# Optimization experiments

Hardware: AMD Instinct MI355X
Metric: run time of the kernel (lower is better)

Reference implementation:

```python
import jax, jax.numpy as jnp
import numpy as np

NR, NQ, NH, NV = 256, 64, 64, 4
B = 8192
NDRAW = 12
# zoneout probabilities from __init__ (applied deterministically, eval-mode expectation)
ZO_IJ, ZO_ID, ZO_GJ, ZO_GD = 0.3, 0.2, 0.3, 0.2


def _lin_init(key, fan_in, fan_out):
    kw, kb = jax.random.split(key)
    s = 1.0 / np.sqrt(fan_in)
    W = jax.random.uniform(kw, (fan_in, fan_out), jnp.float32, -s, s)
    b = jax.random.uniform(kb, (fan_out,), jnp.float32, -s, s)
    return W, b


def setup_inputs() -> dict:
    key = jax.random.key(0)
    ks = jax.random.split(key, 16)
    inp = {"ndraw": NDRAW}
    inp["cnd_repr"] = jax.random.normal(ks[0], (B, NR), jnp.float32)
    inp["qry_jrep"] = jax.random.normal(ks[1], (B, NQ), jnp.float32)
    inp["qry_drep"] = jax.random.normal(ks[2], (B, NQ), jnp.float32)
    inp["qry_v"] = jax.random.normal(ks[3], (B, NV), jnp.float32)
    for n in ["hi_j", "ci_j", "oi_j", "hi_d", "ci_d", "oi_d",
              "hg_j", "cg_j", "og_j", "hg_d", "cg_d", "og_d", "ug_j", "ug_d"]:
        inp[n] = jnp.zeros((B, NH), jnp.float32)
    # LSTM cells: W [in+nh, 4*nh]
    inp["W_ij"], inp["b_ij"] = _lin_init(ks[4], NR + NQ + NH + NH, 4 * NH)
    inp["W_id"], inp["b_id"] = _lin_init(ks[5], NR + NQ + NH + NH, 4 * NH)
    inp["W_gj"], inp["b_gj"] = _lin_init(ks[6], NR + NH + NH, 4 * NH)
    inp["W_gd"], inp["b_gd"] = _lin_init(ks[7], NR + NH + NV + NH, 4 * NH)
    # GaussianFactor heads: nh -> (mean, logv)
    inp["W_poj"], inp["b_poj"] = _lin_init(ks[8], NH, 2 * NH)
    inp["W_pod"], inp["b_pod"] = _lin_init(ks[9], NH, 2 * NH)
    inp["W_prj"], inp["b_prj"] = _lin_init(ks[10], NH, 2 * NH)
    inp["W_prd"], inp["b_prd"] = _lin_init(ks[11], NH, 2 * NH)
    # GeneratorDelta: cat(u, h) -> delta
    inp["W_dj"], inp["b_dj"] = _lin_init(ks[12], 2 * NH, NH)
    inp["W_dd"], inp["b_dd"] = _lin_init(ks[13], 2 * NH, NH)
    return inp


def _lstm(x, h, c, W, b, zo):
    g = jnp.concatenate([x, h], axis=1) @ W + b  # [B, 4*NH]
    i, f, gg, o = jnp.split(g, 4, axis=1)
    i, f, o = jax.nn.sigmoid(i), jax.nn.sigmoid(f), jax.nn.sigmoid(o)
    c_new = f * c + i * jnp.tanh(gg)
    h_new = o * jnp.tanh(c_new)
    # deterministic zoneout (expectation form)
    return zo * h + (1.0 - zo) * h_new, zo * c + (1.0 - zo) * c_new, o


def _gauss_stats(h, W, b):
    s = h @ W + b
    mean, logv = jnp.split(s, 2, axis=1)
    return mean, logv


def _delta(u, h, W, b):
    return jax.nn.leaky_relu(jnp.concatenate([u, h], axis=1) @ W + b)


def _forward(ndraw, cnd_repr, qry_jrep, qry_drep, qry_v,
             hi_j, ci_j, oi_j, hi_d, ci_d, oi_d,
             hg_j, cg_j, og_j, hg_d, cg_d, og_d, ug_j, ug_d,
             W_ij, b_ij, W_id, b_id, W_gj, b_gj, W_gd, b_gd,
             W_poj, b_poj, W_pod, b_pod, W_prj, b_prj, W_prd, b_prd,
             W_dj, b_dj, W_dd, b_dd):
    Bn = cnd_repr.shape[0]
    eps_j = jax.random.normal(jax.random.key(1), (ndraw, Bn, NH), jnp.float32)
    eps_d = jax.random.normal(jax.random.key(2), (ndraw, Bn, NH), jnp.float32)

    def step(carry, eps):
        (hi_j, ci_j, oi_j, hi_d, ci_d, oi_d,
         hg_j, cg_j, og_j, hg_d, cg_d, og_d, ug_j, ug_d) = carry
        ej, ed = eps
        # priors from current generator states (sampled z unused in loop)
        pr_m_j, pr_v_j = _gauss_stats(hg_j, W_prj, b_prj)
        pr_m_d, pr_v_d = _gauss_stats(hg_d, W_prd, b_prd)
        # inference states
        inp_ij = jnp.concatenate([cnd_repr, qry_jrep, hg_j], axis=1)
        inp_id = jnp.concatenate([cnd_repr, qry_drep, hg_d], axis=1)
        hi_j, ci_j, oi_j = _lstm(inp_ij, hi_j, ci_j, W_ij, b_ij, ZO_IJ)
        hi_d, ci_d, oi_d = _lstm(inp_id, hi_d, ci_d, W_id, b_id, ZO_ID)
        # posteriors + reparameterized samples
        po_m_j, po_v_j = _gauss_stats(hi_j, W_poj, b_poj)
        po_m_d, po_v_d = _gauss_stats(hi_d, W_pod, b_pod)
        z_j = po_m_j + jnp.exp(0.5 * po_v_j) * ej
        z_d = po_m_d + jnp.exp(0.5 * po_v_d) * ed
        # generator states
        inp_gj = jnp.concatenate([cnd_repr, z_j], axis=1)
        inp_gd = jnp.concatenate([cnd_repr, z_d, qry_v], axis=1)
        hg_j, cg_j, og_j = _lstm(inp_gj, hg_j, cg_j, W_gj, b_gj, ZO_GJ)
        hg_d, cg_d, og_d = _lstm(inp_gd, hg_d, cg_d, W_gd, b_gd, ZO_GD)
        # additive canvas updates
        ug_j = ug_j + _delta(ug_j, hg_j, W_dj, b_dj)
        ug_d = ug_d + _delta(ug_d, hg_d, W_dd, b_dd)
        carry = (hi_j, ci_j, oi_j, hi_d, ci_d, oi_d,
                 hg_j, cg_j, og_j, hg_d, cg_d, og_d, ug_j, ug_d)
        ys = (pr_m_j, pr_v_j, pr_m_d, pr_v_d, po_m_j, po_v_j, po_m_d, po_v_d)
        return carry, ys

    carry0 = (hi_j, ci_j, oi_j, hi_d, ci_d, oi_d,
              hg_j, cg_j, og_j, hg_d, cg_d, og_d, ug_j, ug_d)
    carry, ys = jax.lax.scan(step, carry0, (eps_j, eps_d))
    ug_j_out, ug_d_out = carry[-2], carry[-1]
    # pack: [2 + 8*ndraw, B, NH] (canvases then per-draw prior/posterior stats)
    out = jnp.concatenate([ug_j_out[None], ug_d_out[None]] + list(ys), axis=0)
    return out


def reference(ndraw, cnd_repr, qry_jrep, qry_drep, qry_v,
              hi_j, ci_j, oi_j, hi_d, ci_d, oi_d,
              hg_j, cg_j, og_j, hg_d, cg_d, og_d, ug_j, ug_d,
              W_ij, b_ij, W_id, b_id, W_gj, b_gj, W_gd, b_gd,
              W_poj, b_poj, W_pod, b_pod, W_prj, b_prj, W_prd, b_prd,
              W_dj, b_dj, W_dd, b_dd):
    return _forward(ndraw, cnd_repr, qry_jrep, qry_drep, qry_v,
                    hi_j, ci_j, oi_j, hi_d, ci_d, oi_d,
                    hg_j, cg_j, og_j, hg_d, cg_d, og_d, ug_j, ug_d,
                    W_ij, b_ij, W_id, b_id, W_gj, b_gj, W_gd, b_gd,
                    W_poj, b_poj, W_pod, b_pod, W_prj, b_prj, W_prd, b_prd,
                    W_dj, b_dj, W_dd, b_dd)
```

## Files before the change

kernel.cpp:

```cpp
#include <hip/hip_runtime.h>
#include <hip/hip_bf16.h>


typedef __attribute__((ext_vector_type(8))) short bf16x8;
typedef __attribute__((ext_vector_type(4))) float f32x4;

#define MFMA(A, Bv, C) __builtin_amdgcn_mfma_f32_16x16x32_bf16(A, Bv, C, 0, 0, 0)

#define FR_WI   0
#define FR_WG   32768
#define FR_WPR  65536
#define FR_WPO  73728
#define FR_WD   81920
#define FR_SIDE 90112

__device__ __forceinline__ unsigned short f2bf(float f) {
  unsigned u = __float_as_uint(f);
  return (unsigned short)((u + 0x7FFFu + ((u >> 16) & 1u)) >> 16);
}
__device__ __forceinline__ unsigned pk2(float a, float b) {
  return (unsigned)f2bf(a) | ((unsigned)f2bf(b) << 16);
}
__device__ __forceinline__ float sigf(float x) {
  return 1.0f / (1.0f + __expf(-x));
}
__device__ __forceinline__ float tanh_f(float x) {
  return 1.0f - 2.0f / (__expf(2.0f * x) + 1.0f);
}

__device__ __forceinline__ float eps_threefry(unsigned seed, unsigned idx) {
  unsigned x0 = 0u, x1 = idx;
  const unsigned ks0 = 0u, ks1 = seed, ks2 = seed ^ 0x1BD11BDAu;
  x0 += ks0; x1 += ks1;
#define TF_R(r) { x0 += x1; x1 = (x1 << (r)) | (x1 >> (32 - (r))); x1 ^= x0; }
  TF_R(13) TF_R(15) TF_R(26) TF_R(6)  x0 += ks1; x1 += ks2 + 1u;
  TF_R(17) TF_R(29) TF_R(16) TF_R(24) x0 += ks2; x1 += ks0 + 2u;
  TF_R(13) TF_R(15) TF_R(26) TF_R(6)  x0 += ks0; x1 += ks1 + 3u;
  TF_R(17) TF_R(29) TF_R(16) TF_R(24) x0 += ks1; x1 += ks2 + 4u;
  TF_R(13) TF_R(15) TF_R(26) TF_R(6)  x0 += ks2; x1 += ks0 + 5u;
#undef TF_R
  unsigned bits = x0 ^ x1;
  unsigned fb = (bits >> 9) | 0x3F800000u;
  const float lo = -0.99999994f;
  float f = __uint_as_float(fb) - 1.0f;
  float u = fmaxf(lo, f * 2.0f + lo);
  float w = -log1pf(-u * u);
  float p;
  if (w < 5.0f) {
    w -= 2.5f;
    p = 2.81022636e-08f;
    p = fmaf(p, w, 3.43273939e-07f);
    p = fmaf(p, w, -3.5233877e-06f);
    p = fmaf(p, w, -4.39150654e-06f);
    p = fmaf(p, w, 0.00021858087f);
    p = fmaf(p, w, -0.00125372503f);
    p = fmaf(p, w, -0.00417768164f);
    p = fmaf(p, w, 0.246640727f);
    p = fmaf(p, w, 1.50140941f);
  } else {
    w = sqrtf(w) - 3.0f;
    p = -0.000200214257f;
    p = fmaf(p, w, 0.000100950558f);
    p = fmaf(p, w, 0.00134934322f);
    p = fmaf(p, w, -0.00367342844f);
    p = fmaf(p, w, 0.00573950773f);
    p = fmaf(p, w, -0.0076224613f);
    p = fmaf(p, w, 0.00943887047f);
    p = fmaf(p, w, 1.00167406f);
    p = fmaf(p, w, 2.83297682f);
  }
  return 1.41421356f * (p * u);
}

__global__ __launch_bounds__(256) void GeRN_prepEps(
    const float* __restrict__ Wij, const float* __restrict__ Wid,
    const float* __restrict__ Wgj, const float* __restrict__ Wgd,
    const float* __restrict__ Wprj, const float* __restrict__ Wprd,
    const float* __restrict__ Wpoj, const float* __restrict__ Wpod,
    const float* __restrict__ Wdj, const float* __restrict__ Wdd,
    unsigned short* __restrict__ frB, unsigned short* __restrict__ sBs,
    float* __restrict__ ebuf, unsigned ndBN)
{
  if (blockIdx.x < 236) {
    const int vb = blockIdx.x * 4 + (threadIdx.x >> 6);
    const int l = threadIdx.x & 63;
    if (vb < 352) {
      const int s = vb / 176;
      int tt = vb % 176;
      const float* W; int ldw, rb, NT, kt, nt; size_t doff;
      if (tt < 64)       { W = s ? Wid : Wij; ldw = 256; NT = 16; kt = tt >> 4; nt = tt & 15;
                           rb = 320 + kt * 32; doff = FR_WI; }
      else if (tt < 128) { tt -= 64; W = s ? Wgd : Wgj; ldw = 256; NT = 16; kt = tt >> 4; nt = tt & 15;
                           rb = (kt < 2) ? 256 + kt * 32 : (s ? 324 : 320) + (kt - 2) * 32; doff = FR_WG; }
      else if (tt < 144) { tt -= 128; W = s ? Wprd : Wprj; ldw = 128; NT = 8; kt = tt >> 3; nt = tt & 7;
                           rb = kt * 32; doff = FR_WPR; }
      else if (tt < 160) { tt -= 144; W = s ? Wpod : Wpoj; ldw = 128; NT = 8; kt = tt >> 3; nt = tt & 7;
                           rb = kt * 32; doff = FR_WPO; }
      else               { tt -= 160; W = s ? Wdd : Wdj; ldw = 64; NT = 4; kt = tt >> 2; nt = tt & 3;
                           rb = (kt < 2) ? kt * 32 : 64 + (kt - 2) * 32; doff = FR_WD; }
      unsigned short* dst = frB + (size_t)s * FR_SIDE + doff
                          + ((size_t)(kt * NT + nt) * 64 + l) * 8;
      const int kk = (l >> 4) * 8;
      const int c = nt * 16 + (l & 15);
      #pragma unroll
      for (int j = 0; j < 8; ++j)
        dst[j] = f2bf(W[(size_t)(rb + kk + j) * ldw + c]);
    } else {
      int bb = vb - 352;
      int mat, base;
      if (bb < 160)      { mat = 0; base = 0; }
      else if (bb < 320) { mat = 1; base = 160; }
      else if (bb < 448) { mat = 2; base = 320; }
      else               { mat = 3; base = 448; }
      int tt = bb - base;
      int kk = tt >> 4, nt = tt & 15;
      const float* W = mat == 0 ? Wij : mat == 1 ? Wid : mat == 2 ? Wgj : Wgd;
      const int c = nt * 16 + (l & 15);
      const int kl0 = (l >> 4) * 8;
      unsigned short* dst = sBs + ((size_t)bb * 64 + l) * 8;
      if (mat == 3 && kk == 8) {
        #pragma unroll
        for (int j = 0; j < 8; ++j) {
          int klo = kl0 + j;
          dst[j] = (klo < 4) ? f2bf(W[(size_t)(320 + klo) * 256 + c]) : (unsigned short)0;
        }
      } else {
        int rb = (kk < 8) ? kk * 32 : 256 + (kk - 8) * 32;
        #pragma unroll
        for (int j = 0; j < 8; ++j)
          dst[j] = f2bf(W[(size_t)(rb + kl0 + j) * 256 + c]);
      }
    }
  } else {
    unsigned j0 = ((blockIdx.x - 236) * 256u + threadIdx.x) * 8u;
    const unsigned total = 2u * ndBN;
    if (j0 >= total) return;
    const unsigned s = (j0 >= ndBN) ? 1u : 0u;
    const unsigned i0 = j0 - s * ndBN;
    const unsigned seed = 1u + s;
    float v[8];
    #pragma unroll
    for (int k = 0; k < 8; ++k) v[k] = eps_threefry(seed, i0 + (unsigned)k);
    float4 a = {v[0], v[1], v[2], v[3]};
    float4 b = {v[4], v[5], v[6], v[7]};
    *(float4*)(ebuf + j0) = a;
    *(float4*)(ebuf + j0 + 4) = b;
  }
}

#define WR_FR(buf, row, c, v) \
  fr[rh][buf][(c) >> 5][((row) & 15) + (((c) >> 3) & 3) * 16][(c) & 7] = f2bf(v)
#define LD_FR(buf, kt) (*(const bf16x8*)&fr[rh][buf][kt][l][0])
#define LD_B(off, kt, nt, NT) \
  (*(const bf16x8*)(FB + (off) + (((kt) * (NT) + (nt)) * 64 + l) * 8))
#define LD_S(idx) (*(const bf16x8*)&sBs[((size_t)(idx) * 64 + l) * 8])
#define LD_WI(kt, nt) (*(const bf16x8*)&wiL[(((kt) * 16 + (nt)) * 64 + l) * 8])
#define LD_WG(kt, nt) (*(const bf16x8*)&wgL[(((kt) * 16 + (nt)) * 64 + l) * 8])
#define LD_A(kt) (*(const bf16x8*)&AsBuf[(((size_t)rh * 11 + (kt)) * 64 + l) * 8])

template<int USE_EPS>
__global__ __launch_bounds__(512, 2) void GeRN_recur(
    const unsigned short* __restrict__ frB,
    const unsigned short* __restrict__ sBs,
    const float* __restrict__ cnd, const float* __restrict__ qjg,
    const float* __restrict__ qdg, const float* __restrict__ qvg,
    const float* __restrict__ bij, const float* __restrict__ bid,
    const float* __restrict__ bgj, const float* __restrict__ bgd,
    const float* __restrict__ bprj, const float* __restrict__ bprd,
    const float* __restrict__ bpoj, const float* __restrict__ bpod,
    const float* __restrict__ bdj,  const float* __restrict__ bdd,
    const float* __restrict__ hi_j0, const float* __restrict__ ci_j0,
    const float* __restrict__ hi_d0, const float* __restrict__ ci_d0,
    const float* __restrict__ hg_j0, const float* __restrict__ cg_j0,
    const float* __restrict__ hg_d0, const float* __restrict__ cg_d0,
    const float* __restrict__ ug_j0, const float* __restrict__ ug_d0,
    const float* __restrict__ eps_buf, unsigned ndBN,
    float* __restrict__ out, int B, int nd)
{
  alignas(16) __shared__ unsigned short fr[2][6][2][64][8];
  alignas(16) __shared__ unsigned short wiL[32768];
  alignas(16) __shared__ unsigned short wgL[32768];
  unsigned short* AsBuf = wgL;

  const int tid = threadIdx.x;
  const int l   = tid & 63;
  const int w   = tid >> 6;
  const int rh  = w >> 2;
  const int ws  = w & 3;
  const int s   = blockIdx.x & 1;
  const int rbk = blockIdx.x >> 1;
  const int r0  = (l >> 4) * 4;
  const int col = ws * 16 + (l & 15);
  const int bbase = rbk * 32 + rh * 16;
  const int bblk  = rbk * 32;
  const size_t BN = (size_t)B * 64;

  const float* hi0 = s ? hi_d0 : hi_j0;  const float* ci0 = s ? ci_d0 : ci_j0;
  const float* hg0 = s ? hg_d0 : hg_j0;  const float* cg0 = s ? cg_d0 : cg_j0;
  const float* ug0 = s ? ug_d0 : ug_j0;
  const float* BPR = s ? bprd : bprj;
  const float* BPO = s ? bpod : bpoj;
  const float* BD  = s ? bdd  : bdj;
  const float* BI  = s ? bid  : bij;
  const float* BG  = s ? bgd  : bgj;
  const float* qq  = s ? qdg  : qjg;
  const unsigned short* FB = frB + (size_t)s * FR_SIDE;

  for (int i = tid; i < 32 * 44; i += 512) {
    int r = i / 44, kc = i % 44;
    int rhh = r >> 4, rr = r & 15;
    float v[8];
    if (kc < 32) {
      const float4* p = (const float4*)&cnd[(size_t)(bblk + r) * 256 + kc * 8];
      float4 x0 = p[0], x1 = p[1];
      v[0] = x0.x; v[1] = x0.y; v[2] = x0.z; v[3] = x0.w;
      v[4] = x1.x; v[5] = x1.y; v[6] = x1.z; v[7] = x1.w;
    } else if (kc < 40) {
      const float4* p = (const float4*)&qq[(size_t)(bblk + r) * 64 + (kc - 32) * 8];
      float4 x0 = p[0], x1 = p[1];
      v[0] = x0.x; v[1] = x0.y; v[2] = x0.z; v[3] = x0.w;
      v[4] = x1.x; v[5] = x1.y; v[6] = x1.z; v[7] = x1.w;
    } else if (kc == 40 && s) {
      #pragma unroll
      for (int j = 0; j < 8; ++j) v[j] = (j < 4) ? qvg[(size_t)(bblk + r) * 4 + j] : 0.0f;
    } else {
      #pragma unroll
      for (int j = 0; j < 8; ++j) v[j] = 0.0f;
    }
    int kt = kc >> 2;
    int lane = rr + (kc & 3) * 16;
    uint4 wq;
    wq.x = pk2(v[0], v[1]); wq.y = pk2(v[2], v[3]);
    wq.z = pk2(v[4], v[5]); wq.w = pk2(v[6], v[7]);
    *(uint4*)&AsBuf[(((size_t)rhh * 11 + kt) * 64 + lane) * 8] = wq;
  }
  __syncthreads();

  f32x4 preI[4], preG[4];
  {
    const int ktB_I = s ? 160 : 0;
    const int ktB_G = s ? 448 : 320;
    const int ktN_G = s ? 9 : 8;
    #pragma unroll
    for (int g = 0; g < 4; ++g) {
      float bi = BI[g * 64 + col];
      float bg = BG[g * 64 + col];
      f32x4 vi = {bi, bi, bi, bi};
      f32x4 vg = {bg, bg, bg, bg};
      preI[g] = vi; preG[g] = vg;
    }
    #pragma unroll
    for (int kk = 0; kk < 10; ++kk) {
      bf16x8 a = LD_A(kk);
      #pragma unroll
      for (int g = 0; g < 4; ++g)
        preI[g] = MFMA(a, LD_S(ktB_I + kk * 16 + g * 4 + ws), preI[g]);
    }
    for (int kk = 0; kk < ktN_G; ++kk) {
      int ktA = (kk < 8) ? kk : 10;
      bf16x8 a = LD_A(ktA);
      #pragma unroll
      for (int g = 0; g < 4; ++g)
        preG[g] = MFMA(a, LD_S(ktB_G + kk * 16 + g * 4 + ws), preG[g]);
    }
  }

  float hi_[4], ci_[4], hg_[4], cg_[4], u_[4];
  #pragma unroll
  for (int r = 0; r < 4; ++r) {
    size_t gi = (size_t)(bbase + r0 + r) * 64 + col;
    hi_[r] = hi0[gi]; ci_[r] = ci0[gi];
    hg_[r] = hg0[gi]; cg_[r] = cg0[gi];
    u_[r]  = ug0[gi];
  }
  const float bprm = BPR[col], bprv = BPR[64 + col];
  const float bpom = BPO[col], bpov = BPO[64 + col];
  const float bd   = BD[col];

  #pragma unroll
  for (int r = 0; r < 4; ++r) {
    WR_FR(0, r0 + r, col, hi_[r]);
    WR_FR(2, r0 + r, col, hg_[r]);
    WR_FR(4, r0 + r, col, u_[r]);
  }
  __syncthreads();

  {
    const uint4* srcI = (const uint4*)(FB + FR_WI);
    uint4* dI = (uint4*)wiL;
    for (int i = tid; i < 4096; i += 512) dI[i] = srcI[i];
    const uint4* srcG = (const uint4*)(FB + FR_WG);
    uint4* dG = (uint4*)wgL;
    for (int i = tid; i < 4096; i += 512) dG[i] = srcG[i];
  }
  __syncthreads();

  const float zo = s ? 0.2f : 0.3f, zo1 = 1.0f - zo;

  const unsigned gi0 = (unsigned)((bbase + r0) * 64 + col);
  float* o_prm = out + (size_t)(2 + (2 * s) * nd) * BN + gi0;
  float* o_prv = out + (size_t)(2 + (2 * s + 1) * nd) * BN + gi0;
  float* o_pom = out + (size_t)(2 + (4 + 2 * s) * nd) * BN + gi0;
  float* o_pov = out + (size_t)(2 + (5 + 2 * s) * nd) * BN + gi0;
  unsigned e0 = gi0;
  const unsigned BNu = (unsigned)BN;
  const unsigned eseed = 1u + (unsigned)s;
  const float* ep = USE_EPS ? (eps_buf + (size_t)s * ndBN + gi0) : (const float*)0;

  for (int t = 0; t < nd; ++t) {
    const int cb = t & 1;
    float epre[4];
    if (USE_EPS) {
      #pragma unroll
      for (int r = 0; r < 4; ++r) epre[r] = ep[r * 64];
    }
    bf16x8 a_hg0 = LD_FR(2, 0), a_hg1 = LD_FR(2, 1);
    bf16x8 a_hi0 = LD_FR(cb, 0), a_hi1 = LD_FR(cb, 1);

    {
      f32x4 am = {bprm, bprm, bprm, bprm};
      f32x4 av = {bprv, bprv, bprv, bprv};
      am = MFMA(a_hg0, LD_B(FR_WPR, 0, ws, 8), am);
      am = MFMA(a_hg1, LD_B(FR_WPR, 1, ws, 8), am);
      av = MFMA(a_hg0, LD_B(FR_WPR, 0, ws + 4, 8), av);
      av = MFMA(a_hg1, LD_B(FR_WPR, 1, ws + 4, 8), av);
      #pragma unroll
      for (int r = 0; r < 4; ++r) {
        o_prm[r * 64] = am[r];
        o_prv[r * 64] = av[r];
      }
    }
    {
      f32x4 acc[4];
      #pragma unroll
      for (int g = 0; g < 4; ++g) acc[g] = preI[g];
      #pragma unroll
      for (int g = 0; g < 4; ++g) {
        acc[g] = MFMA(a_hg0, LD_WI(0, g * 4 + ws), acc[g]);
        acc[g] = MFMA(a_hg1, LD_WI(1, g * 4 + ws), acc[g]);
        acc[g] = MFMA(a_hi0, LD_WI(2, g * 4 + ws), acc[g]);
        acc[g] = MFMA(a_hi1, LD_WI(3, g * 4 + ws), acc[g]);
      }
      #pragma unroll
      for (int r = 0; r < 4; ++r) {
        float ig = sigf(acc[0][r]), fg = sigf(acc[1][r]);
        float gg = tanh_f(acc[2][r]), og = sigf(acc[3][r]);
        float cn = fmaf(fg, ci_[r], ig * gg);
        float hn = og * tanh_f(cn);
        hi_[r] = fmaf(zo, hi_[r], zo1 * hn);
        ci_[r] = fmaf(zo, ci_[r], zo1 * cn);
        WR_FR(cb ^ 1, r0 + r, col, hi_[r]);
      }
    }
    __syncthreads();

    {
      bf16x8 a0 = LD_FR(cb ^ 1, 0), a1 = LD_FR(cb ^ 1, 1);
      f32x4 am = {bpom, bpom, bpom, bpom};
      f32x4 av = {bpov, bpov, bpov, bpov};
      am = MFMA(a0, LD_B(FR_WPO, 0, ws, 8), am);
      am = MFMA(a1, LD_B(FR_WPO, 1, ws, 8), am);
      av = MFMA(a0, LD_B(FR_WPO, 0, ws + 4, 8), av);
      av = MFMA(a1, LD_B(FR_WPO, 1, ws + 4, 8), av);
      #pragma unroll
      for (int r = 0; r < 4; ++r) {
        o_pom[r * 64] = am[r];
        o_pov[r * 64] = av[r];
        float e = USE_EPS ? epre[r] : eps_threefry(eseed, e0 + r * 64);
        float z = fmaf(__expf(0.5f * av[r]), e, am[r]);
        WR_FR(3, r0 + r, col, z);
      }
    }
    __syncthreads();

    {
      bf16x8 az0 = LD_FR(3, 0), az1 = LD_FR(3, 1);
      f32x4 acc[4];
      #pragma unroll
      for (int g = 0; g < 4; ++g) acc[g] = preG[g];
      #pragma unroll
      for (int g = 0; g < 4; ++g) {
        acc[g] = MFMA(az0,   LD_WG(0, g * 4 + ws), acc[g]);
        acc[g] = MFMA(az1,   LD_WG(1, g * 4 + ws), acc[g]);
        acc[g] = MFMA(a_hg0, LD_WG(2, g * 4 + ws), acc[g]);
        acc[g] = MFMA(a_hg1, LD_WG(3, g * 4 + ws), acc[g]);
      }
      #pragma unroll
      for (int r = 0; r < 4; ++r) {
        float ig = sigf(acc[0][r]), fg = sigf(acc[1][r]);
        float gg = tanh_f(acc[2][r]), og = sigf(acc[3][r]);
        float cn = fmaf(fg, cg_[r], ig * gg);
        float hn = og * tanh_f(cn);
        hg_[r] = fmaf(zo, hg_[r], zo1 * hn);
        cg_[r] = fmaf(zo, cg_[r], zo1 * cn);
        WR_FR(2, r0 + r, col, hg_[r]);
      }
    }
    __syncthreads();

    {
      bf16x8 au0 = LD_FR(4 + cb, 0), au1 = LD_FR(4 + cb, 1);
      bf16x8 ah0 = LD_FR(2, 0), ah1 = LD_FR(2, 1);
      f32x4 acc = {bd, bd, bd, bd};
      acc = MFMA(au0, LD_B(FR_WD, 0, ws, 4), acc);
      acc = MFMA(au1, LD_B(FR_WD, 1, ws, 4), acc);
      acc = MFMA(ah0, LD_B(FR_WD, 2, ws, 4), acc);
      acc = MFMA(ah1, LD_B(FR_WD, 3, ws, 4), acc);
      #pragma unroll
      for (int r = 0; r < 4; ++r) {
        float a = acc[r];
        float d = a > 0.0f ? a : 0.01f * a;
        u_[r] += d;
        WR_FR(4 + (cb ^ 1), r0 + r, col, u_[r]);
      }
    }
    __syncthreads();

    o_prm += BN; o_prv += BN; o_pom += BN; o_pov += BN;
    e0 += BNu;
    if (USE_EPS) ep += BN;
  }

  #pragma unroll
  for (int r = 0; r < 4; ++r) {
    size_t gi = (size_t)(bbase + r0 + r) * 64 + col;
    out[(size_t)s * BN + gi] = u_[r];
  }
}

extern "C" void kernel_launch(void* const* d_in, const int* in_sizes, int n_in,
                              void* d_out, int out_size, void* d_ws, size_t ws_size,
                              hipStream_t stream)
{
  const float* cnd = (const float*)d_in[1];
  const float* qj  = (const float*)d_in[2];
  const float* qd  = (const float*)d_in[3];
  const float* qv  = (const float*)d_in[4];
  const float* hi_j0 = (const float*)d_in[5];
  const float* ci_j0 = (const float*)d_in[6];
  const float* hi_d0 = (const float*)d_in[8];
  const float* ci_d0 = (const float*)d_in[9];
  const float* hg_j0 = (const float*)d_in[11];
  const float* cg_j0 = (const float*)d_in[12];
  const float* hg_d0 = (const float*)d_in[14];
  const float* cg_d0 = (const float*)d_in[15];
  const float* ug_j0 = (const float*)d_in[17];
  const float* ug_d0 = (const float*)d_in[18];
  const float* Wij = (const float*)d_in[19]; const float* bij = (const float*)d_in[20];
  const float* Wid = (const float*)d_in[21]; const float* bid = (const float*)d_in[22];
  const float* Wgj = (const float*)d_in[23]; const float* bgj = (const float*)d_in[24];
  const float* Wgd = (const float*)d_in[25]; const float* bgd = (const float*)d_in[26];
  const float* Wpoj = (const float*)d_in[27]; const float* bpoj = (const float*)d_in[28];
  const float* Wpod = (const float*)d_in[29]; const float* bpod = (const float*)d_in[30];
  const float* Wprj = (const float*)d_in[31]; const float* bprj = (const float*)d_in[32];
  const float* Wprd = (const float*)d_in[33]; const float* bprd = (const float*)d_in[34];
  const float* Wdj = (const float*)d_in[35]; const float* bdj = (const float*)d_in[36];
  const float* Wdd = (const float*)d_in[37]; const float* bdd = (const float*)d_in[38];

  const int B = in_sizes[1] / 256;
  const int slots = out_size / (B * 64);
  const int nd = (slots - 2) / 8;

  unsigned short* frB = (unsigned short*)d_ws;
  unsigned short* sBs = frB + 2 * FR_SIDE;
  size_t epsOff = (size_t)2 * FR_SIDE * 2 + (size_t)592 * 512 * 2;
  epsOff = (epsOff + 255) & ~(size_t)255;
  const unsigned ndBN = (unsigned)((size_t)nd * B * 64);
  float* epsBuf = (float*)((char*)d_ws + epsOff);
  const bool useEps = ws_size >= epsOff + (size_t)2 * ndBN * 4;
  float* out = (float*)d_out;

  const int epsBlocks = useEps ? (int)((2u * ndBN + 2047u) / 2048u) : 0;
  GeRN_prepEps<<<236 + epsBlocks, 256, 0, stream>>>(
      Wij, Wid, Wgj, Wgd, Wprj, Wprd, Wpoj, Wpod, Wdj, Wdd, frB, sBs,
      epsBuf, ndBN);
  if (useEps) {
    GeRN_recur<1><<<2 * (B / 32), 512, 0, stream>>>(
        frB, sBs, cnd, qj, qd, qv, bij, bid, bgj, bgd,
        bprj, bprd, bpoj, bpod, bdj, bdd,
        hi_j0, ci_j0, hi_d0, ci_d0, hg_j0, cg_j0, hg_d0, cg_d0, ug_j0, ug_d0,
        epsBuf, ndBN, out, B, nd);
  } else {
    GeRN_recur<0><<<2 * (B / 32), 512, 0, stream>>>(
        frB, sBs, cnd, qj, qd, qv, bij, bid, bgj, bgd,
        bprj, bprd, bpoj, bpod, bdj, bdd,
        hi_j0, ci_j0, hi_d0, ci_d0, hg_j0, cg_j0, hg_d0, cg_d0, ug_j0, ug_d0,
        (const float*)0, ndBN, out, B, nd);
  }
}
```

Measured before the change: 191.2 us.

## Process 64 batch rows per block with two column tiles per wave

```diff
diff --git a/kernel.cpp b/kernel.cpp
--- a/kernel.cpp
+++ b/kernel.cpp
@@ -149,14 +149,14 @@
 }
 
 #define WR_FR(buf, row, c, v) \
-  fr[rh][buf][(c) >> 5][((row) & 15) + (((c) >> 3) & 3) * 16][(c) & 7] = f2bf(v)
-#define LD_FR(buf, kt) (*(const bf16x8*)&fr[rh][buf][kt][l][0])
+  fr[rq][buf][(c) >> 5][((row) & 15) + (((c) >> 3) & 3) * 16][(c) & 7] = f2bf(v)
+#define LD_FR(buf, kt) (*(const bf16x8*)&fr[rq][buf][kt][l][0])
 #define LD_B(off, kt, nt, NT) \
   (*(const bf16x8*)(FB + (off) + (((kt) * (NT) + (nt)) * 64 + l) * 8))
 #define LD_S(idx) (*(const bf16x8*)&sBs[((size_t)(idx) * 64 + l) * 8])
 #define LD_WI(kt, nt) (*(const bf16x8*)&wiL[(((kt) * 16 + (nt)) * 64 + l) * 8])
 #define LD_WG(kt, nt) (*(const bf16x8*)&wgL[(((kt) * 16 + (nt)) * 64 + l) * 8])
-#define LD_A(kt) (*(const bf16x8*)&AsBuf[(((size_t)rh * 11 + (kt)) * 64 + l) * 8])
+#define LD_A(kt) (*(const bf16x8*)&AsBuf[(((size_t)rq * 11 + (kt)) * 64 + l) * 8])
 
 template<int USE_EPS>
 __global__ __launch_bounds__(512, 2) void GeRN_recur(
@@ -177,7 +177,7 @@
     const float* __restrict__ eps_buf, unsigned ndBN,
     float* __restrict__ out, int B, int nd)
 {
-  alignas(16) __shared__ unsigned short fr[2][6][2][64][8];
+  alignas(16) __shared__ unsigned short fr[4][4][2][64][8];
   alignas(16) __shared__ unsigned short wiL[32768];
   alignas(16) __shared__ unsigned short wgL[32768];
   unsigned short* AsBuf = wgL;
@@ -185,14 +185,14 @@
   const int tid = threadIdx.x;
   const int l   = tid & 63;
   const int w   = tid >> 6;
-  const int rh  = w >> 2;
-  const int ws  = w & 3;
+  const int rq  = w >> 1;
+  const int ws  = w & 1;
   const int s   = blockIdx.x & 1;
   const int rbk = blockIdx.x >> 1;
   const int r0  = (l >> 4) * 4;
-  const int col = ws * 16 + (l & 15);
-  const int bbase = rbk * 32 + rh * 16;
-  const int bblk  = rbk * 32;
+  const int col0 = ws * 32 + (l & 15);
+  const int bbase = rbk * 64 + rq * 16;
+  const int bblk  = rbk * 64;
   const size_t BN = (size_t)B * 64;
 
   const float* hi0 = s ? hi_d0 : hi_j0;  const float* ci0 = s ? ci_d0 : ci_j0;
@@ -206,9 +206,9 @@
   const float* qq  = s ? qdg  : qjg;
   const unsigned short* FB = frB + (size_t)s * FR_SIDE;
 
-  for (int i = tid; i < 32 * 44; i += 512) {
+  for (int i = tid; i < 64 * 44; i += 512) {
     int r = i / 44, kc = i % 44;
-    int rhh = r >> 4, rr = r & 15;
+    int rqq = r >> 4, rr = r & 15;
     float v[8];
     if (kc < 32) {
       const float4* p = (const float4*)&cnd[(size_t)(bblk + r) * 256 + kc * 8];
@@ -232,57 +232,71 @@
     uint4 wq;
     wq.x = pk2(v[0], v[1]); wq.y = pk2(v[2], v[3]);
     wq.z = pk2(v[4], v[5]); wq.w = pk2(v[6], v[7]);
-    *(uint4*)&AsBuf[(((size_t)rhh * 11 + kt) * 64 + lane) * 8] = wq;
+    *(uint4*)&AsBuf[(((size_t)rqq * 11 + kt) * 64 + lane) * 8] = wq;
   }
   __syncthreads();
 
-  f32x4 preI[4], preG[4];
+  f32x4 preI[4][2], preG[4][2];
   {
     const int ktB_I = s ? 160 : 0;
     const int ktB_G = s ? 448 : 320;
     const int ktN_G = s ? 9 : 8;
     #pragma unroll
-    for (int g = 0; g < 4; ++g) {
-      float bi = BI[g * 64 + col];
-      float bg = BG[g * 64 + col];
-      f32x4 vi = {bi, bi, bi, bi};
-      f32x4 vg = {bg, bg, bg, bg};
-      preI[g] = vi; preG[g] = vg;
-    }
+    for (int g = 0; g < 4; ++g)
+      #pragma unroll
+      for (int c = 0; c < 2; ++c) {
+        float bi = BI[g * 64 + col0 + c * 16];
+        float bg = BG[g * 64 + col0 + c * 16];
+        f32x4 vi = {bi, bi, bi, bi};
+        f32x4 vg = {bg, bg, bg, bg};
+        preI[g][c] = vi; preG[g][c] = vg;
+      }
     #pragma unroll
     for (int kk = 0; kk < 10; ++kk) {
       bf16x8 a = LD_A(kk);
       #pragma unroll
       for (int g = 0; g < 4; ++g)
-        preI[g] = MFMA(a, LD_S(ktB_I + kk * 16 + g * 4 + ws), preI[g]);
+        #pragma unroll
+        for (int c = 0; c < 2; ++c)
+          preI[g][c] = MFMA(a, LD_S(ktB_I + kk * 16 + g * 4 + ws * 2 + c), preI[g][c]);
     }
     for (int kk = 0; kk < ktN_G; ++kk) {
       int ktA = (kk < 8) ? kk : 10;
       bf16x8 a = LD_A(ktA);
       #pragma unroll
       for (int g = 0; g < 4; ++g)
-        preG[g] = MFMA(a, LD_S(ktB_G + kk * 16 + g * 4 + ws), preG[g]);
-    }
-  }
-
-  float hi_[4], ci_[4], hg_[4], cg_[4], u_[4];
+        #pragma unroll
+        for (int c = 0; c < 2; ++c)
+          preG[g][c] = MFMA(a, LD_S(ktB_G + kk * 16 + g * 4 + ws * 2 + c), preG[g][c]);
+    }
+  }
+
+  float hi_[2][4], ci_[2][4], hg_[2][4], cg_[2][4], u_[2][4];
   #pragma unroll
-  for (int r = 0; r < 4; ++r) {
-    size_t gi = (size_t)(bbase + r0 + r) * 64 + col;
-    hi_[r] = hi0[gi]; ci_[r] = ci0[gi];
-    hg_[r] = hg0[gi]; cg_[r] = cg0[gi];
-    u_[r]  = ug0[gi];
-  }
-  const float bprm = BPR[col], bprv = BPR[64 + col];
-  const float bpom = BPO[col], bpov = BPO[64 + col];
-  const float bd   = BD[col];
-
+  for (int c = 0; c < 2; ++c)
+    #pragma unroll
+    for (int r = 0; r < 4; ++r) {
+      size_t gi = (size_t)(bbase + r0 + r) * 64 + col0 + c * 16;
+      hi_[c][r] = hi0[gi]; ci_[c][r] = ci0[gi];
+      hg_[c][r] = hg0[gi]; cg_[c][r] = cg0[gi];
+      u_[c][r]  = ug0[gi];
+    }
+  float bprm[2], bprv[2], bpom[2], bpov[2], bd[2];
   #pragma unroll
-  for (int r = 0; r < 4; ++r) {
-    WR_FR(0, r0 + r, col, hi_[r]);
-    WR_FR(2, r0 + r, col, hg_[r]);
-    WR_FR(4, r0 + r, col, u_[r]);
-  }
+  for (int c = 0; c < 2; ++c) {
+    bprm[c] = BPR[col0 + c * 16]; bprv[c] = BPR[64 + col0 + c * 16];
+    bpom[c] = BPO[col0 + c * 16]; bpov[c] = BPO[64 + col0 + c * 16];
+    bd[c]   = BD[col0 + c * 16];
+  }
+
+  #pragma unroll
+  for (int c = 0; c < 2; ++c)
+    #pragma unroll
+    for (int r = 0; r < 4; ++r) {
+      WR_FR(0, r0 + r, col0 + c * 16, hi_[c][r]);
+      WR_FR(1, r0 + r, col0 + c * 16, hg_[c][r]);
+      WR_FR(3, r0 + r, col0 + c * 16, u_[c][r]);
+    }
   __syncthreads();
 
   {
@@ -297,7 +311,7 @@
 
   const float zo = s ? 0.2f : 0.3f, zo1 = 1.0f - zo;
 
-  const unsigned gi0 = (unsigned)((bbase + r0) * 64 + col);
+  const unsigned gi0 = (unsigned)((bbase + r0) * 64 + col0);
   float* o_prm = out + (size_t)(2 + (2 * s) * nd) * BN + gi0;
   float* o_prv = out + (size_t)(2 + (2 * s + 1) * nd) * BN + gi0;
   float* o_pom = out + (size_t)(2 + (4 + 2 * s) * nd) * BN + gi0;
@@ -308,113 +322,141 @@
   const float* ep = USE_EPS ? (eps_buf + (size_t)s * ndBN + gi0) : (const float*)0;
 
   for (int t = 0; t < nd; ++t) {
-    const int cb = t & 1;
-    float epre[4];
+    float epre[2][4];
     if (USE_EPS) {
       #pragma unroll
-      for (int r = 0; r < 4; ++r) epre[r] = ep[r * 64];
-    }
-    bf16x8 a_hg0 = LD_FR(2, 0), a_hg1 = LD_FR(2, 1);
-    bf16x8 a_hi0 = LD_FR(cb, 0), a_hi1 = LD_FR(cb, 1);
+      for (int c = 0; c < 2; ++c)
+        #pragma unroll
+        for (int r = 0; r < 4; ++r) epre[c][r] = ep[r * 64 + c * 16];
+    }
+    bf16x8 a_hg0 = LD_FR(1, 0), a_hg1 = LD_FR(1, 1);
+    bf16x8 a_hi0 = LD_FR(0, 0), a_hi1 = LD_FR(0, 1);
 
     {
-      f32x4 am = {bprm, bprm, bprm, bprm};
-      f32x4 av = {bprv, bprv, bprv, bprv};
-      am = MFMA(a_hg0, LD_B(FR_WPR, 0, ws, 8), am);
-      am = MFMA(a_hg1, LD_B(FR_WPR, 1, ws, 8), am);
-      av = MFMA(a_hg0, LD_B(FR_WPR, 0, ws + 4, 8), av);
-      av = MFMA(a_hg1, LD_B(FR_WPR, 1, ws + 4, 8), av);
-      #pragma unroll
-      for (int r = 0; r < 4; ++r) {
-        o_prm[r * 64] = am[r];
-        o_prv[r * 64] = av[r];
+      #pragma unroll
+      for (int c = 0; c < 2; ++c) {
+        f32x4 am = {bprm[c], bprm[c], bprm[c], bprm[c]};
+        f32x4 av = {bprv[c], bprv[c], bprv[c], bprv[c]};
+        am = MFMA(a_hg0, LD_B(FR_WPR, 0, ws * 2 + c, 8), am);
+        am = MFMA(a_hg1, LD_B(FR_WPR, 1, ws * 2 + c, 8), am);
+        av = MFMA(a_hg0, LD_B(FR_WPR, 0, 4 + ws * 2 + c, 8), av);
+        av = MFMA(a_hg1, LD_B(FR_WPR, 1, 4 + ws * 2 + c, 8), av);
+        #pragma unroll
+        for (int r = 0; r < 4; ++r) {
+          o_prm[r * 64 + c * 16] = am[r];
+          o_prv[r * 64 + c * 16] = av[r];
+        }
       }
     }
     {
-      f32x4 acc[4];
-      #pragma unroll
-      for (int g = 0; g < 4; ++g) acc[g] = preI[g];
-      #pragma unroll
-      for (int g = 0; g < 4; ++g) {
-        acc[g] = MFMA(a_hg0, LD_WI(0, g * 4 + ws), acc[g]);
-        acc[g] = MFMA(a_hg1, LD_WI(1, g * 4 + ws), acc[g]);
-        acc[g] = MFMA(a_hi0, LD_WI(2, g * 4 + ws), acc[g]);
-        acc[g] = MFMA(a_hi1, LD_WI(3, g * 4 + ws), acc[g]);
+      f32x4 acc[4][2];
+      #pragma unroll
+      for (int g = 0; g < 4; ++g)
+        #pragma unroll
+        for (int c = 0; c < 2; ++c) acc[g][c] = preI[g][c];
+      #pragma unroll
+      for (int g = 0; g < 4; ++g)
+        #pragma unroll
+        for (int c = 0; c < 2; ++c) {
+          acc[g][c] = MFMA(a_hg0, LD_WI(0, g * 4 + ws * 2 + c), acc[g][c]);
+          acc[g][c] = MFMA(a_hg1, LD_WI(1, g * 4 + ws * 2 + c), acc[g][c]);
+          acc[g][c] = MFMA(a_hi0, LD_WI(2, g * 4 + ws * 2 + c), acc[g][c]);
+          acc[g][c] = MFMA(a_hi1, LD_WI(3, g * 4 + ws * 2 + c), acc[g][c]);
+        }
+      #pragma unroll
+      for (int c = 0; c < 2; ++c)
+        #pragma unroll
+        for (int r = 0; r < 4; ++r) {
+          float ig = sigf(acc[0][c][r]), fg = sigf(acc[1][c][r]);
+          float gg = tanh_f(acc[2][c][r]), og = sigf(acc[3][c][r]);
+          float cn = fmaf(fg, ci_[c][r], ig * gg);
+          float hn = og * tanh_f(cn);
+          hi_[c][r] = fmaf(zo, hi_[c][r], zo1 * hn);
+          ci_[c][r] = fmaf(zo, ci_[c][r], zo1 * cn);
+        }
+      __syncthreads();
+      #pragma unroll
+      for (int c = 0; c < 2; ++c)
+        #pragma unroll
+        for (int r = 0; r < 4; ++r)
+          WR_FR(0, r0 + r, col0 + c * 16, hi_[c][r]);
+    }
+    __syncthreads();
+
+    {
+      bf16x8 a0 = LD_FR(0, 0), a1 = LD_FR(0, 1);
+      #pragma unroll
+      for (int c = 0; c < 2; ++c) {
+        f32x4 am = {bpom[c], bpom[c], bpom[c], bpom[c]};
+        f32x4 av = {bpov[c], bpov[c], bpov[c], bpov[c]};
+        am = MFMA(a0, LD_B(FR_WPO, 0, ws * 2 + c, 8), am);
+        am = MFMA(a1, LD_B(FR_WPO, 1, ws * 2 + c, 8), am);
+        av = MFMA(a0, LD_B(FR_WPO, 0, 4 + ws * 2 + c, 8), av);
+        av = MFMA(a1, LD_B(FR_WPO, 1, 4 + ws * 2 + c, 8), av);
+        #pragma unroll
+        for (int r = 0; r < 4; ++r) {
+          o_pom[r * 64 + c * 16] = am[r];
+          o_pov[r * 64 + c * 16] = av[r];
+          float e = USE_EPS ? epre[c][r]
+                            : eps_threefry(eseed, e0 + r * 64 + c * 16);
+          float z = fmaf(__expf(0.5f * av[r]), e, am[r]);
+          WR_FR(2, r0 + r, col0 + c * 16, z);
+        }
       }
-      #pragma unroll
-      for (int r = 0; r < 4; ++r) {
-        float ig = sigf(acc[0][r]), fg = sigf(acc[1][r]);
-        float gg = tanh_f(acc[2][r]), og = sigf(acc[3][r]);
-        float cn = fmaf(fg, ci_[r], ig * gg);
-        float hn = og * tanh_f(cn);
-        hi_[r] = fmaf(zo, hi_[r], zo1 * hn);
-        ci_[r] = fmaf(zo, ci_[r], zo1 * cn);
-        WR_FR(cb ^ 1, r0 + r, col, hi_[r]);
+    }
+    __syncthreads();
+
+    {
+      bf16x8 az0 = LD_FR(2, 0), az1 = LD_FR(2, 1);
+      f32x4 acc[4][2];
+      #pragma unroll
+      for (int g = 0; g < 4; ++g)
+        #pragma unroll
+        for (int c = 0; c < 2; ++c) acc[g][c] = preG[g][c];
+      #pragma unroll
+      for (int g = 0; g < 4; ++g)
+        #pragma unroll
+        for (int c = 0; c < 2; ++c) {
+          acc[g][c] = MFMA(az0,   LD_WG(0, g * 4 + ws * 2 + c), acc[g][c]);
+          acc[g][c] = MFMA(az1,   LD_WG(1, g * 4 + ws * 2 + c), acc[g][c]);
+          acc[g][c] = MFMA(a_hg0, LD_WG(2, g * 4 + ws * 2 + c), acc[g][c]);
+          acc[g][c] = MFMA(a_hg1, LD_WG(3, g * 4 + ws * 2 + c), acc[g][c]);
+        }
+      #pragma unroll
+      for (int c = 0; c < 2; ++c)
+        #pragma unroll
+        for (int r = 0; r < 4; ++r) {
+          float ig = sigf(acc[0][c][r]), fg = sigf(acc[1][c][r]);
+          float gg = tanh_f(acc[2][c][r]), og = sigf(acc[3][c][r]);
+          float cn = fmaf(fg, cg_[c][r], ig * gg);
+          float hn = og * tanh_f(cn);
+          hg_[c][r] = fmaf(zo, hg_[c][r], zo1 * hn);
+          cg_[c][r] = fmaf(zo, cg_[c][r], zo1 * cn);
+          WR_FR(1, r0 + r, col0 + c * 16, hg_[c][r]);
+        }
+    }
+    __syncthreads();
+
+    {
+      bf16x8 au0 = LD_FR(3, 0), au1 = LD_FR(3, 1);
+      bf16x8 ah0 = LD_FR(1, 0), ah1 = LD_FR(1, 1);
+      __syncthreads();
+      #pragma unroll
+      for (int c = 0; c < 2; ++c) {
+        f32x4 acc = {bd[c], bd[c], bd[c], bd[c]};
+        acc = MFMA(au0, LD_B(FR_WD, 0, ws * 2 + c, 4), acc);
+        acc = MFMA(au1, LD_B(FR_WD, 1, ws * 2 + c, 4), acc);
+        acc = MFMA(ah0, LD_B(FR_WD, 2, ws * 2 + c, 4), acc);
+        acc = MFMA(ah1, LD_B(FR_WD, 3, ws * 2 + c, 4), acc);
+        #pragma unroll
+        for (int r = 0; r < 4; ++r) {
+          float a = acc[r];
+          float d = a > 0.0f ? a : 0.01f * a;
+          u_[c][r] += d;
+          WR_FR(3, r0 + r, col0 + c * 16, u_[c][r]);
+        }
       }
     }
-    __syncthreads();
-
-    {
-      bf16x8 a0 = LD_FR(cb ^ 1, 0), a1 = LD_FR(cb ^ 1, 1);
-      f32x4 am = {bpom, bpom, bpom, bpom};
-      f32x4 av = {bpov, bpov, bpov, bpov};
-      am = MFMA(a0, LD_B(FR_WPO, 0, ws, 8), am);
-      am = MFMA(a1, LD_B(FR_WPO, 1, ws, 8), am);
-      av = MFMA(a0, LD_B(FR_WPO, 0, ws + 4, 8), av);
-      av = MFMA(a1, LD_B(FR_WPO, 1, ws + 4, 8), av);
-      #pragma unroll
-      for (int r = 0; r < 4; ++r) {
-        o_pom[r * 64] = am[r];
-        o_pov[r * 64] = av[r];
-        float e = USE_EPS ? epre[r] : eps_threefry(eseed, e0 + r * 64);
-        float z = fmaf(__expf(0.5f * av[r]), e, am[r]);
-        WR_FR(3, r0 + r, col, z);
-      }
-    }
-    __syncthreads();
-
-    {
-      bf16x8 az0 = LD_FR(3, 0), az1 = LD_FR(3, 1);
-      f32x4 acc[4];
-      #pragma unroll
-      for (int g = 0; g < 4; ++g) acc[g] = preG[g];
-      #pragma unroll
-      for (int g = 0; g < 4; ++g) {
-        acc[g] = MFMA(az0,   LD_WG(0, g * 4 + ws), acc[g]);
-        acc[g] = MFMA(az1,   LD_WG(1, g * 4 + ws), acc[g]);
-        acc[g] = MFMA(a_hg0, LD_WG(2, g * 4 + ws), acc[g]);
-        acc[g] = MFMA(a_hg1, LD_WG(3, g * 4 + ws), acc[g]);
-      }
-      #pragma unroll
-      for (int r = 0; r < 4; ++r) {
-        float ig = sigf(acc[0][r]), fg = sigf(acc[1][r]);
-        float gg = tanh_f(acc[2][r]), og = sigf(acc[3][r]);
-        float cn = fmaf(fg, cg_[r], ig * gg);
-        float hn = og * tanh_f(cn);
-        hg_[r] = fmaf(zo, hg_[r], zo1 * hn);
-        cg_[r] = fmaf(zo, cg_[r], zo1 * cn);
-        WR_FR(2, r0 + r, col, hg_[r]);
-      }
-    }
-    __syncthreads();
-
-    {
-      bf16x8 au0 = LD_FR(4 + cb, 0), au1 = LD_FR(4 + cb, 1);
-      bf16x8 ah0 = LD_FR(2, 0), ah1 = LD_FR(2, 1);
-      f32x4 acc = {bd, bd, bd, bd};
-      acc = MFMA(au0, LD_B(FR_WD, 0, ws, 4), acc);
-      acc = MFMA(au1, LD_B(FR_WD, 1, ws, 4), acc);
-      acc = MFMA(ah0, LD_B(FR_WD, 2, ws, 4), acc);
-      acc = MFMA(ah1, LD_B(FR_WD, 3, ws, 4), acc);
-      #pragma unroll
-      for (int r = 0; r < 4; ++r) {
-        float a = acc[r];
-        float d = a > 0.0f ? a : 0.01f * a;
-        u_[r] += d;
-        WR_FR(4 + (cb ^ 1), r0 + r, col, u_[r]);
-      }
-    }
-    __syncthreads();
 
     o_prm += BN; o_prv += BN; o_pom += BN; o_pov += BN;
     e0 += BNu;
@@ -422,10 +464,12 @@
   }
 
   #pragma unroll
-  for (int r = 0; r < 4; ++r) {
-    size_t gi = (size_t)(bbase + r0 + r) * 64 + col;
-    out[(size_t)s * BN + gi] = u_[r];
-  }
+  for (int c = 0; c < 2; ++c)
+    #pragma unroll
+    for (int r = 0; r < 4; ++r) {
+      size_t gi = (size_t)(bbase + r0 + r) * 64 + col0 + c * 16;
+      out[(size_t)s * BN + gi] = u_[c][r];
+    }
 }
 
 extern "C" void kernel_launch(void* const* d_in, const int* in_sizes, int n_in,
@@ -475,13 +519,13 @@
       Wij, Wid, Wgj, Wgd, Wprj, Wprd, Wpoj, Wpod, Wdj, Wdd, frB, sBs,
       epsBuf, ndBN);
   if (useEps) {
-    GeRN_recur<1><<<2 * (B / 32), 512, 0, stream>>>(
+    GeRN_recur<1><<<2 * (B / 64), 512, 0, stream>>>(
         frB, sBs, cnd, qj, qd, qv, bij, bid, bgj, bgd,
         bprj, bprd, bpoj, bpod, bdj, bdd,
         hi_j0, ci_j0, hi_d0, ci_d0, hg_j0, cg_j0, hg_d0, cg_d0, ug_j0, ug_d0,
         epsBuf, ndBN, out, B, nd);
   } else {
-    GeRN_recur<0><<<2 * (B / 32), 512, 0, stream>>>(
+    GeRN_recur<0><<<2 * (B / 64), 512, 0, stream>>>(
         frB, sBs, cnd, qj, qd, qv, bij, bid, bgj, bgd,
         bprj, bprd, bpoj, bpod, bdj, bdd,
         hi_j0, ci_j0, hi_d0, ci_d0, hg_j0, cg_j0, hg_d0, cg_d0, ug_j0, ug_d0,
```

Result: slower. 243.3 us (+27.2%).
